# Kernel optimization log

Hardware: AMD Instinct MI355X
Metric: run time of the kernel (lower is better)

The kernel has to match this reference:

```python
import jax, jax.numpy as jnp
import numpy as np

SEQ_LEN = 2048
EMBED_DIM = 1024
NUM_HEADS = 16
DIM_HEAD = EMBED_DIM // NUM_HEADS
BATCH = 4


def setup_inputs() -> dict:
    key = jax.random.key(0)
    k1, k2, k3 = jax.random.split(key, 3)
    x = jax.random.normal(k1, (SEQ_LEN, BATCH, EMBED_DIM), dtype=jnp.float32)
    weight_qkv = jax.random.normal(k2, (3 * EMBED_DIM, EMBED_DIM), dtype=jnp.float32) * (EMBED_DIM ** -0.5)
    weight_out = jax.random.normal(k3, (EMBED_DIM, EMBED_DIM), dtype=jnp.float32) * (EMBED_DIM ** -0.5)
    # causal mask: True where attention is DISALLOWED (strict upper triangle)
    mask = ~jnp.tril(jnp.ones((SEQ_LEN, SEQ_LEN), dtype=bool))[None, None]  # [1,1,L,L]
    return {"x": x, "weight_qkv": weight_qkv, "weight_out": weight_out, "mask": mask}


def reference(x, weight_qkv, weight_out, mask):
    L, N, E = x.shape
    H, Dh = NUM_HEADS, DIM_HEAD
    scale = Dh ** -0.5
    qkv = x @ weight_qkv.T                       # [L, N, 3E]
    q, k, v = jnp.split(qkv, 3, axis=-1)         # each [L, N, E]
    # [L, N, E] -> [N*H, L, Dh]
    def to_heads(t):
        return t.reshape(L, N * H, Dh).transpose(1, 0, 2)
    q, k, v = to_heads(q) * scale, to_heads(k), to_heads(v)
    attn = jnp.einsum('bld,bmd->blm', q, k)      # [N*H, L, L]
    attn = attn.reshape(N, H, L, L)
    attn = jnp.where(mask, jnp.float32(-100000.0), attn)
    attn = jax.nn.softmax(attn.reshape(N * H, L, L), axis=-1)
    out = jnp.einsum('blm,bmd->bld', attn, v)    # [N*H, L, Dh]
    out = out.transpose(1, 0, 2).reshape(L, N, E)
    return out @ weight_out.T
```

## Files before the change

### kernel.cpp

```cpp
#include <hip/hip_runtime.h>
#include <hip/hip_bf16.h>
#include <stdint.h>

constexpr int L  = 2048;
constexpr int NB = 4;
constexpr int E  = 1024;
constexpr int H  = 16;
constexpr int M  = L * NB;
constexpr int K  = E;
constexpr int QKV_LD = 3 * E;

typedef float  f32x4  __attribute__((ext_vector_type(4)));
typedef __bf16 bf16x4 __attribute__((ext_vector_type(4)));
typedef __bf16 bf16x8 __attribute__((ext_vector_type(8)));

#define AS1 __attribute__((address_space(1)))
#define AS3 __attribute__((address_space(3)))

static __device__ __forceinline__ void gl_lds16(const void* g, void* l) {
  __builtin_amdgcn_global_load_lds((const AS1 uint32_t*)g, (AS3 uint32_t*)l, 16, 0, 0);
}

__global__ __launch_bounds__(256)
void cvt_f32_bf16(const float* __restrict__ in, __bf16* __restrict__ out, int n4) {
  const int i = blockIdx.x * blockDim.x + threadIdx.x;
  if (i < n4) {
    const f32x4 v = ((const f32x4*)in)[i];
    bf16x4 o;
#pragma unroll
    for (int j = 0; j < 4; j++) o[j] = (__bf16)v[j];
    ((bf16x4*)out)[i] = o;
  }
}

template<int NC, typename OutT>
__global__ __launch_bounds__(256)
void gemm_bt(const __bf16* __restrict__ A, const __bf16* __restrict__ B,
             OutT* __restrict__ C) {
  constexpr int BK = 64;
  __shared__ char lds[2 * 128 * BK * 2];
  char* aL = lds;
  char* bL = lds + 128 * BK * 2;

  const int t    = threadIdx.x;
  const int lane = t & 63;
  const int w    = t >> 6;
  const int g    = lane >> 4;
  const int c    = lane & 15;

  const int rowBase = blockIdx.y * 128;
  const int colBase = blockIdx.x * 128;

  const int srow = t >> 3;
  const int scb  = (t & 7) * 16;
  const int ssw  = scb ^ ((srow & 7) << 4);

  const char* aSrcBase = (const char*)(A + (size_t)(rowBase + srow) * K) + ssw;
  const char* bSrcBase = (const char*)(B + (size_t)(colBase + srow) * K) + ssw;

  f32x4 acc[4][4];
#pragma unroll
  for (int i = 0; i < 4; i++)
#pragma unroll
    for (int j = 0; j < 4; j++) acc[i][j] = f32x4{0.f, 0.f, 0.f, 0.f};

  const int wr = (w >> 1) * 64;
  const int wc = (w & 1) * 64;

  for (int k0 = 0; k0 < K; k0 += BK) {
    __syncthreads();
#pragma unroll
    for (int q = 0; q < 4; q++) {
      gl_lds16(aSrcBase + (size_t)2 * k0 + (size_t)q * 32 * K * 2, aL + q * 4096 + t * 16);
      gl_lds16(bSrcBase + (size_t)2 * k0 + (size_t)q * 32 * K * 2, bL + q * 4096 + t * 16);
    }
    __syncthreads();

    bf16x8 af[4][2], bfR[4][2];
#pragma unroll
    for (int mi = 0; mi < 4; mi++) {
      const int row = wr + mi * 16 + c;
      const int sw  = (row & 7) << 4;
#pragma unroll
      for (int ks = 0; ks < 2; ks++)
        af[mi][ks] = *(const bf16x8*)(aL + row * 128 + ((ks * 64 + g * 16) ^ sw));
    }
#pragma unroll
    for (int ni = 0; ni < 4; ni++) {
      const int row = wc + ni * 16 + c;
      const int sw  = (row & 7) << 4;
#pragma unroll
      for (int ks = 0; ks < 2; ks++)
        bfR[ni][ks] = *(const bf16x8*)(bL + row * 128 + ((ks * 64 + g * 16) ^ sw));
    }
#pragma unroll
    for (int mi = 0; mi < 4; mi++)
#pragma unroll
      for (int ni = 0; ni < 4; ni++)
#pragma unroll
        for (int ks = 0; ks < 2; ks++)
          acc[mi][ni] = __builtin_amdgcn_mfma_f32_16x16x32_bf16(
              af[mi][ks], bfR[ni][ks], acc[mi][ni], 0, 0, 0);
  }

#pragma unroll
  for (int mi = 0; mi < 4; mi++)
#pragma unroll
    for (int ni = 0; ni < 4; ni++)
#pragma unroll
      for (int r = 0; r < 4; r++) {
        const int row = rowBase + wr + mi * 16 + g * 4 + r;
        const int col = colBase + wc + ni * 16 + c;
        C[(size_t)row * NC + col] = (OutT)acc[mi][ni][r];
      }
}

__global__ __launch_bounds__(256)
void transpose_v(const __bf16* __restrict__ qkv, __bf16* __restrict__ vT) {
  __shared__ char tile[64 * 160];
  const int lt = blockIdx.x;
  const int bh = blockIdx.y;
  const int n  = bh >> 4, h = bh & 15;
  const int t  = threadIdx.x;
  const int r8 = t >> 3;
  const int c8 = (t & 7) * 8;

#pragma unroll
  for (int q2 = 0; q2 < 2; q2++) {
    const int l = q2 * 32 + r8;
    const bf16x8 v = *(const bf16x8*)(qkv + (size_t)((lt * 64 + l) * 4 + n) * QKV_LD +
                                      2 * E + h * 64 + c8);
    *(bf16x8*)(tile + l * 160 + ((c8 * 2) ^ (((l >> 3) & 7) << 4))) = v;
  }
  __syncthreads();
#pragma unroll
  for (int q2 = 0; q2 < 2; q2++) {
    const int d = q2 * 32 + r8;
    bf16x8 o;
#pragma unroll
    for (int i = 0; i < 8; i++) {
      const int l = c8 + i;
      o[i] = *(const __bf16*)(tile + l * 160 + ((d * 2) ^ (((l >> 3) & 7) << 4)));
    }
    *(bf16x8*)(vT + ((size_t)bh * 64 + d) * 2048 + lt * 64 + c8) = o;
  }
}

__global__ __launch_bounds__(256)
void attn_kernel(const __bf16* __restrict__ qkv, const __bf16* __restrict__ vT,
                 __bf16* __restrict__ out) {
  const int qx = blockIdx.x;
  const int b  = blockIdx.y;
  const int n  = b >> 4;
  const int h  = b & 15;

  __shared__ char kl[2][64 * 128];
  __shared__ char vl[2][64 * 128];
  __shared__ char pl[4][16 * 128];

  const int t    = threadIdx.x;
  const int lane = t & 63;
  const int w    = t >> 6;
  const int g    = lane >> 4;
  const int c    = lane & 15;

  const int srow = t >> 3;
  const int scb  = (t & 7) * 16;
  const int kssw = scb ^ ((srow & 7) << 4);

  constexpr float QSCALE = 0.125f * 1.4426950408889634f;

  char* pw = pl[w];
  const int qloc = w * 16 + c;

  int cur = 0;

  for (int pass = 0; pass < 2; ++pass) {
    const int qt = pass ? 31 - qx : qx;

    bf16x8 qa0, qa1;
    {
      const int qrow = qt * 64 + qloc;
      const __bf16* qp = qkv + (size_t)(qrow * 4 + n) * QKV_LD + h * 64;
      qa0 = *(const bf16x8*)(qp + g * 8);
      qa1 = *(const bf16x8*)(qp + 32 + g * 8);
#pragma unroll
      for (int i = 0; i < 8; i++) {
        qa0[i] = (__bf16)((float)qa0[i] * QSCALE);
        qa1[i] = (__bf16)((float)qa1[i] * QSCALE);
      }
    }

    float m_c = -3e38f, l_c = 0.f;
    f32x4 o[4];
#pragma unroll
    for (int ni = 0; ni < 4; ni++) o[ni] = f32x4{0.f, 0.f, 0.f, 0.f};

#pragma unroll
    for (int q2 = 0; q2 < 2; q2++) {
      const int kvrow = q2 * 32 + srow;
      gl_lds16((const char*)(qkv + (size_t)(kvrow * 4 + n) * QKV_LD + E + h * 64) + kssw,
               kl[cur] + q2 * 4096 + t * 16);
      gl_lds16((const char*)(vT + ((size_t)b * 64 + q2 * 32 + srow) * 2048) + kssw,
               vl[cur] + q2 * 4096 + t * 16);
    }

    for (int kt = 0; kt <= qt; ++kt) {
      __syncthreads();

      if (kt < qt) {
        const int nx = kt + 1;
#pragma unroll
        for (int q2 = 0; q2 < 2; q2++) {
          const int kvrow = nx * 64 + q2 * 32 + srow;
          gl_lds16((const char*)(qkv + (size_t)(kvrow * 4 + n) * QKV_LD + E + h * 64) + kssw,
                   kl[cur ^ 1] + q2 * 4096 + t * 16);
          const int vd = q2 * 32 + srow;
          gl_lds16((const char*)(vT + ((size_t)b * 64 + vd) * 2048 + nx * 64) + kssw,
                   vl[cur ^ 1] + q2 * 4096 + t * 16);
        }
      }
      __builtin_amdgcn_sched_barrier(0);

      const char* klc = kl[cur];
      const char* vlc = vl[cur];

      f32x4 s[4];
#pragma unroll
      for (int ni = 0; ni < 4; ni++) s[ni] = f32x4{0.f, 0.f, 0.f, 0.f};
      __builtin_amdgcn_s_setprio(1);
#pragma unroll
      for (int ni = 0; ni < 4; ni++) {
        const int row = ni * 16 + c;
        const int sw  = (row & 7) << 4;
        const bf16x8 kb0 = *(const bf16x8*)(klc + row * 128 + ((g * 16) ^ sw));
        const bf16x8 kb1 = *(const bf16x8*)(klc + row * 128 + ((64 + g * 16) ^ sw));
        s[ni] = __builtin_amdgcn_mfma_f32_16x16x32_bf16(kb0, qa0, s[ni], 0, 0, 0);
        s[ni] = __builtin_amdgcn_mfma_f32_16x16x32_bf16(kb1, qa1, s[ni], 0, 0, 0);
      }
      __builtin_amdgcn_s_setprio(0);

      const bool lastTile = (kt == qt);
      float rmax = -3e38f;
#pragma unroll
      for (int ni = 0; ni < 4; ni++)
#pragma unroll
        for (int r = 0; r < 4; r++) {
          float v = s[ni][r];
          if (lastTile && (ni * 16 + g * 4 + r > qloc)) v = -3e38f;
          s[ni][r] = v;
          rmax = fmaxf(rmax, v);
        }
      rmax = fmaxf(rmax, __shfl_xor(rmax, 16));
      rmax = fmaxf(rmax, __shfl_xor(rmax, 32));

      if (__any(rmax > m_c + 8.f)) {
        const float mnew  = fmaxf(m_c, rmax);
        const float alpha = exp2f(m_c - mnew);
        l_c *= alpha;
#pragma unroll
        for (int r = 0; r < 4; r++) {
          const float ar = __shfl(alpha, g * 4 + r);
#pragma unroll
          for (int ni = 0; ni < 4; ni++) o[ni][r] *= ar;
        }
        m_c = mnew;
      }

      float rsum = 0.f;
#pragma unroll
      for (int ni = 0; ni < 4; ni++)
#pragma unroll
        for (int r = 0; r < 4; r++) {
          const float e = exp2f(s[ni][r] - m_c);
          s[ni][r] = e;
          rsum += e;
        }
      rsum += __shfl_xor(rsum, 16);
      rsum += __shfl_xor(rsum, 32);
      l_c += rsum;

#pragma unroll
      for (int ni = 0; ni < 4; ni++) {
        bf16x4 pk;
#pragma unroll
        for (int r = 0; r < 4; r++) pk[r] = (__bf16)s[ni][r];
        *(bf16x4*)(pw + c * 128 + ((ni * 32 + g * 8) ^ ((c & 7) << 4))) = pk;
      }
      bf16x8 pa[2];
      {
        const int sw = (c & 7) << 4;
        pa[0] = *(const bf16x8*)(pw + c * 128 + ((g * 16) ^ sw));
        pa[1] = *(const bf16x8*)(pw + c * 128 + ((64 + g * 16) ^ sw));
      }
      __builtin_amdgcn_s_setprio(1);
#pragma unroll
      for (int ni = 0; ni < 4; ni++) {
        const int row = ni * 16 + c;
        const int sw  = (row & 7) << 4;
        const bf16x8 vb0 = *(const bf16x8*)(vlc + row * 128 + ((g * 16) ^ sw));
        const bf16x8 vb1 = *(const bf16x8*)(vlc + row * 128 + ((64 + g * 16) ^ sw));
        o[ni] = __builtin_amdgcn_mfma_f32_16x16x32_bf16(pa[0], vb0, o[ni], 0, 0, 0);
        o[ni] = __builtin_amdgcn_mfma_f32_16x16x32_bf16(pa[1], vb1, o[ni], 0, 0, 0);
      }
      __builtin_amdgcn_s_setprio(0);

      cur ^= 1;
    }

#pragma unroll
    for (int r = 0; r < 4; r++) {
      const float lr   = __shfl(l_c, g * 4 + r);
      const float inv  = 1.f / lr;
      const int   qrow = qt * 64 + w * 16 + g * 4 + r;
#pragma unroll
      for (int ni = 0; ni < 4; ni++) {
        const size_t off = (size_t)(qrow * 4 + n) * E + h * 64 + ni * 16 + c;
        out[off] = (__bf16)(o[ni][r] * inv);
      }
    }
  }
}

extern "C" void kernel_launch(void* const* d_in, const int* in_sizes, int n_in,
                              void* d_out, int out_size, void* d_ws, size_t ws_size,
                              hipStream_t stream) {
  const float* x    = (const float*)d_in[0];
  const float* wqkv = (const float*)d_in[1];
  const float* wout = (const float*)d_in[2];

  char* ws = (char*)d_ws;
  __bf16* x_bf    = (__bf16*)ws;                         ws += (size_t)M * E * 2;
  __bf16* wqkv_bf = (__bf16*)ws;                         ws += (size_t)QKV_LD * E * 2;
  __bf16* wout_bf = (__bf16*)ws;                         ws += (size_t)E * E * 2;
  __bf16* qkv     = (__bf16*)ws;                         ws += (size_t)M * QKV_LD * 2;
  __bf16* attno   = (__bf16*)ws;
  __bf16* vT      = x_bf;
  float*  outp    = (float*)d_out;

  cvt_f32_bf16<<<(M * E / 4) / 256, 256, 0, stream>>>(x, x_bf, M * E / 4);
  cvt_f32_bf16<<<(QKV_LD * E / 4) / 256, 256, 0, stream>>>(wqkv, wqkv_bf, QKV_LD * E / 4);
  cvt_f32_bf16<<<(E * E / 4) / 256, 256, 0, stream>>>(wout, wout_bf, E * E / 4);

  gemm_bt<QKV_LD, __bf16><<<dim3(QKV_LD / 128, M / 128), 256, 0, stream>>>(x_bf, wqkv_bf, qkv);
  transpose_v<<<dim3(L / 64, NB * H), 256, 0, stream>>>(qkv, vT);
  attn_kernel<<<dim3(16, NB * H), 256, 0, stream>>>(qkv, vT, attno);
  gemm_bt<E, float><<<dim3(E / 128, M / 128), 256, 0, stream>>>(attno, wout_bf, outp);
}
```

Measured before the change: 204.4 us.

## Swizzle GEMM block order across XCDs, reorder attention grid, prefetch next pass KV

The GEMM remaps the linear workgroup index so that consecutive blocks, which are dealt round-robin across the eight XCDs, land on contiguous tiles. This aims to improve L2 reuse per XCD. The attention grid is transposed so heads vary fastest, and the last K/V tile iteration now prefetches tile 0 for the second query pass, overlapping that load with compute. The causal mask is split out of the max-reduction loop. The prefetch relies on the pass structure being correct, which adds some risk.

```diff
diff --git a/kernel.cpp b/kernel.cpp
--- a/kernel.cpp
+++ b/kernel.cpp
@@ -48,8 +48,15 @@
   const int g    = lane >> 4;
   const int c    = lane & 15;
 
-  const int rowBase = blockIdx.y * 128;
-  const int colBase = blockIdx.x * 128;
+  const int nwg = gridDim.x * gridDim.y;
+  const int lin = blockIdx.x + gridDim.x * blockIdx.y;
+  const int q8  = nwg >> 3;
+  const int swz = (lin & 7) * q8 + (lin >> 3);
+  const int bx  = swz % gridDim.x;
+  const int by  = swz / gridDim.x;
+
+  const int rowBase = by * 128;
+  const int colBase = bx * 128;
 
   const int srow = t >> 3;
   const int scb  = (t & 7) * 16;
@@ -149,8 +156,8 @@
 __global__ __launch_bounds__(256)
 void attn_kernel(const __bf16* __restrict__ qkv, const __bf16* __restrict__ vT,
                  __bf16* __restrict__ out) {
-  const int qx = blockIdx.x;
-  const int b  = blockIdx.y;
+  const int b  = blockIdx.x;
+  const int qx = blockIdx.y;
   const int n  = b >> 4;
   const int h  = b & 15;
 
@@ -196,20 +203,23 @@
 #pragma unroll
     for (int ni = 0; ni < 4; ni++) o[ni] = f32x4{0.f, 0.f, 0.f, 0.f};
 
-#pragma unroll
-    for (int q2 = 0; q2 < 2; q2++) {
-      const int kvrow = q2 * 32 + srow;
-      gl_lds16((const char*)(qkv + (size_t)(kvrow * 4 + n) * QKV_LD + E + h * 64) + kssw,
-               kl[cur] + q2 * 4096 + t * 16);
-      gl_lds16((const char*)(vT + ((size_t)b * 64 + q2 * 32 + srow) * 2048) + kssw,
-               vl[cur] + q2 * 4096 + t * 16);
+    if (pass == 0) {
+#pragma unroll
+      for (int q2 = 0; q2 < 2; q2++) {
+        const int kvrow = q2 * 32 + srow;
+        gl_lds16((const char*)(qkv + (size_t)(kvrow * 4 + n) * QKV_LD + E + h * 64) + kssw,
+                 kl[cur] + q2 * 4096 + t * 16);
+        gl_lds16((const char*)(vT + ((size_t)b * 64 + q2 * 32 + srow) * 2048) + kssw,
+                 vl[cur] + q2 * 4096 + t * 16);
+      }
     }
 
     for (int kt = 0; kt <= qt; ++kt) {
       __syncthreads();
 
-      if (kt < qt) {
-        const int nx = kt + 1;
+      const bool lastTile = (kt == qt);
+      if (!lastTile || pass == 0) {
+        const int nx = lastTile ? 0 : kt + 1;
 #pragma unroll
         for (int q2 = 0; q2 < 2; q2++) {
           const int kvrow = nx * 64 + q2 * 32 + srow;
@@ -240,17 +250,19 @@
       }
       __builtin_amdgcn_s_setprio(0);
 
-      const bool lastTile = (kt == qt);
+      if (lastTile) {
+#pragma unroll
+        for (int ni = 0; ni < 4; ni++)
+#pragma unroll
+          for (int r = 0; r < 4; r++)
+            if (ni * 16 + g * 4 + r > qloc) s[ni][r] = -3e38f;
+      }
+
       float rmax = -3e38f;
 #pragma unroll
       for (int ni = 0; ni < 4; ni++)
 #pragma unroll
-        for (int r = 0; r < 4; r++) {
-          float v = s[ni][r];
-          if (lastTile && (ni * 16 + g * 4 + r > qloc)) v = -3e38f;
-          s[ni][r] = v;
-          rmax = fmaxf(rmax, v);
-        }
+        for (int r = 0; r < 4; r++) rmax = fmaxf(rmax, s[ni][r]);
       rmax = fmaxf(rmax, __shfl_xor(rmax, 16));
       rmax = fmaxf(rmax, __shfl_xor(rmax, 32));
 
@@ -344,6 +356,6 @@
 
   gemm_bt<QKV_LD, __bf16><<<dim3(QKV_LD / 128, M / 128), 256, 0, stream>>>(x_bf, wqkv_bf, qkv);
   transpose_v<<<dim3(L / 64, NB * H), 256, 0, stream>>>(qkv, vT);
-  attn_kernel<<<dim3(16, NB * H), 256, 0, stream>>>(qkv, vT, attno);
+  attn_kernel<<<dim3(NB * H, 16), 256, 0, stream>>>(qkv, vT, attno);
   gemm_bt<E, float><<<dim3(E / 128, M / 128), 256, 0, stream>>>(attno, wout_bf, outp);
 }
```

After: 196.0 us. 1.04x faster.
